# Kernel optimization log

Hardware: AMD Instinct MI355X
Metric: run time of the kernel (lower is better)

The kernel has to match this reference:

```python
import jax, jax.numpy as jnp
import numpy as np

TEMPERATURE = 8.0  # sqrt(head_dim=64)


def setup_inputs() -> dict:
    key = jax.random.key(0)
    ks = jax.random.split(key, 6)
    B, H, S, D = 8, 8, 1024, 64
    shp = (B, H, S, D)
    names = ["q_r", "q_i", "k_r", "k_i", "v_r", "v_i"]
    return {n: jax.random.normal(k, shp, dtype=jnp.float32) for n, k in zip(names, ks)}


def _mag_minmax_norm(attn):
    """cvnn.MagMinMaxNorm(dim=-1): min-max normalize the magnitude along the
    last axis while preserving phase: x * (|x| - min) / ((max - min) * |x|)."""
    mag = jnp.abs(attn)                              # [B,H,Sq,Sk] real
    mn = jnp.min(mag, axis=-1, keepdims=True)
    mx = jnp.max(mag, axis=-1, keepdims=True)
    return attn * ((mag - mn) / ((mx - mn) * mag))


def reference(q_r, q_i, k_r, k_i, v_r, v_i):
    q = jax.lax.complex(q_r, q_i)
    k = jax.lax.complex(k_r, k_i)
    v = jax.lax.complex(v_r, v_i)
    # complex QK^T with temperature scaling
    attn = jnp.einsum("bhqd,bhkd->bhqk", q / TEMPERATURE, k)
    attn = _mag_minmax_norm(attn)
    # dropout is identity at inference (eval mode)
    out = jnp.einsum("bhqk,bhkd->bhqd", attn, v)
    # return real/imag stacked: [2, B, H, S, D]
    return jnp.stack([out.real, out.imag])
```

## Files before the change

### kernel.cpp

```cpp
#include <hip/hip_runtime.h>
#include <math.h>

typedef unsigned short ushort_t;
typedef __attribute__((ext_vector_type(8))) short short8;
typedef __attribute__((ext_vector_type(4))) float f32x4;
typedef __attribute__((ext_vector_type(4))) int int4v;
typedef __attribute__((ext_vector_type(4))) unsigned short ushort4v;

constexpr int S = 1024, D = 64, BH = 64;
constexpr int HALF = BH * S * D;
constexpr int KROW = 72;
constexpr int VROW = 40;
constexpr int TILE_USH = 2 * 32 * KROW + 2 * 64 * VROW;
constexpr size_t WS_NEED = (size_t)BH * 32 * TILE_USH * 2;

#define MFMA16(a, b, c) __builtin_amdgcn_mfma_f32_16x16x32_bf16(a, b, c, 0, 0, 0)

__device__ __forceinline__ ushort_t f2bf(float f) {
  unsigned u = __float_as_uint(f);
  u += 0x7fff + ((u >> 16) & 1);
  return (ushort_t)(u >> 16);
}

__global__ __launch_bounds__(256)
void prepass_kernel(const float* __restrict__ kr, const float* __restrict__ ki,
                    const float* __restrict__ vr, const float* __restrict__ vi,
                    ushort_t* __restrict__ ws) {
  __shared__ float tmp2[32 * 65];
  const int t = threadIdx.x;
  const int tile = blockIdx.x;
  const size_t gbase = (size_t)tile * (32 * D);
  ushort_t* wst = ws + (size_t)tile * TILE_USH;

  const int k = t >> 3, d0 = (t & 7) * 8;
  {
    const float* kp[2] = {kr, ki};
#pragma unroll
    for (int c = 0; c < 2; ++c) {
      const float* src = kp[c] + gbase + k * D + d0;
      float4 a = *(const float4*)src;
      float4 b = *(const float4*)(src + 4);
      ushort4v w0 = {f2bf(a.x), f2bf(a.y), f2bf(a.z), f2bf(a.w)};
      ushort4v w1 = {f2bf(b.x), f2bf(b.y), f2bf(b.z), f2bf(b.w)};
      ushort_t* dst = wst + c * (32 * KROW) + k * KROW + d0;
      *(ushort4v*)dst = w0;
      *(ushort4v*)(dst + 4) = w1;
    }
  }
  const float* vp[2] = {vr, vi};
  for (int c = 0; c < 2; ++c) {
    if (c) __syncthreads();
    {
      const float* src = vp[c] + gbase + k * D + d0;
      float4 a = *(const float4*)src;
      float4 b = *(const float4*)(src + 4);
      *(float4*)&tmp2[k * 65 + d0] = a;
      *(float4*)&tmp2[k * 65 + d0 + 4] = b;
    }
    __syncthreads();
    const int d = t >> 2, k0 = (t & 3) * 8;
    float v[8];
#pragma unroll
    for (int j = 0; j < 8; ++j) v[j] = tmp2[(k0 + j) * 65 + d];
    ushort4v o0 = {f2bf(v[0]), f2bf(v[1]), f2bf(v[2]), f2bf(v[3])};
    ushort4v o1 = {f2bf(v[4]), f2bf(v[5]), f2bf(v[6]), f2bf(v[7])};
    ushort_t* dst = wst + 2 * (32 * KROW) + c * (64 * VROW) + d * VROW + k0;
    *(ushort4v*)dst = o0;
    *(ushort4v*)(dst + 4) = o1;
  }
}

__global__ __launch_bounds__(256, 2)
void cvattn_mfma(const float* __restrict__ gq_r, const float* __restrict__ gq_i,
                 const ushort_t* __restrict__ ws, float* __restrict__ gout) {
  __shared__ __attribute__((aligned(16))) char smem[39936];
  ushort_t* sB = (ushort_t*)smem;
  ushort_t* sP = (ushort_t*)(smem + 19456);
  ushort_t* sQ = (ushort_t*)(smem + 19456);

  const int t = threadIdx.x;
  const int lane = t & 63, wave = t >> 6;
  const int m = lane & 15, quad = lane >> 4;
  const int qt = blockIdx.x, bh = blockIdx.y;
  const size_t base = (size_t)bh * (S * D);

  {
    const float* qr = gq_r + base + (size_t)qt * (64 * D);
    const float* qi = gq_i + base + (size_t)qt * (64 * D);
#pragma unroll
    for (int i = 0; i < 4; ++i) {
      int e = (i * 256 + t) * 4;
      int q = e >> 6, d = e & 63;
      float4 a = *(const float4*)(qr + e);
      float4 b = *(const float4*)(qi + e);
      ushort4v wa = {f2bf(a.x), f2bf(a.y), f2bf(a.z), f2bf(a.w)};
      ushort4v wb = {f2bf(b.x), f2bf(b.y), f2bf(b.z), f2bf(b.w)};
      *(ushort4v*)&sQ[q * KROW + d] = wa;
      *(ushort4v*)&sQ[64 * KROW + q * KROW + d] = wb;
    }
  }
  __syncthreads();

  short8 fQr[2], fQi[2], fQin[2];
  {
    const int qrow = wave * 16 + m;
#pragma unroll
    for (int dc = 0; dc < 2; ++dc) {
      fQr[dc] = *(const short8*)&sQ[qrow * KROW + dc * 32 + quad * 8];
      fQi[dc] = *(const short8*)&sQ[64 * KROW + qrow * KROW + dc * 32 + quad * 8];
      fQin[dc] = fQi[dc] ^ (short)0x8000;
    }
  }

  f32x4 aAr[4] = {}, aAi[4] = {}, aUr[4] = {}, aUi[4] = {};
  float mn4[4] = {1e30f, 1e30f, 1e30f, 1e30f};
  float mx4[4] = {0.f, 0.f, 0.f, 0.f};

  ushort_t* pw = sP + wave * 2560;
  const ushort_t* wsrc = ws + (size_t)bh * 32 * TILE_USH;

  int4v pre[5];
#pragma unroll
  for (int i = 0; i < 5; ++i) {
    int idx = i * 256 + t;
    if (idx < 1216) pre[i] = *(const int4v*)(wsrc + idx * 8);
  }

  for (int kb = 0; kb < 32; ++kb) {
    __syncthreads();
#pragma unroll
    for (int i = 0; i < 5; ++i) {
      int idx = i * 256 + t;
      if (idx < 1216) *(int4v*)(smem + idx * 16) = pre[i];
    }
    if (kb + 1 < 32) {
      const ushort_t* g = wsrc + (size_t)(kb + 1) * TILE_USH;
#pragma unroll
      for (int i = 0; i < 5; ++i) {
        int idx = i * 256 + t;
        if (idx < 1216) pre[i] = *(const int4v*)(g + idx * 8);
      }
    }
    __syncthreads();

#pragma unroll
    for (int ks = 0; ks < 2; ++ks) {
      const int krow = ks * 16 + m;
      short8 fKr0 = *(const short8*)&sB[krow * KROW + quad * 8];
      short8 fKr1 = *(const short8*)&sB[krow * KROW + 32 + quad * 8];
      short8 fKi0 = *(const short8*)&sB[2304 + krow * KROW + quad * 8];
      short8 fKi1 = *(const short8*)&sB[2304 + krow * KROW + 32 + quad * 8];
      f32x4 cSr = {}, cSi = {};
      cSr = MFMA16(fQr[0], fKr0, cSr);
      cSr = MFMA16(fQr[1], fKr1, cSr);
      cSr = MFMA16(fQin[0], fKi0, cSr);
      cSr = MFMA16(fQin[1], fKi1, cSr);
      cSi = MFMA16(fQr[0], fKi0, cSi);
      cSi = MFMA16(fQr[1], fKi1, cSi);
      cSi = MFMA16(fQi[0], fKr0, cSi);
      cSi = MFMA16(fQi[1], fKr1, cSi);
      const int pcol = ((ks * 2 + (m >> 3)) ^ quad) * 8 + (m & 7);
#pragma unroll
      for (int r = 0; r < 4; ++r) {
        float sr = cSr[r], si = cSi[r];
        float t2 = sr * sr + si * si;
        float rq = __builtin_amdgcn_rsqf(t2);
        mn4[r] = fminf(mn4[r], t2);
        mx4[r] = fmaxf(mx4[r], t2);
        const int off = (quad * 4 + r) * VROW + pcol;
        pw[off] = f2bf(sr);
        pw[640 + off] = f2bf(si);
        pw[1280 + off] = f2bf(sr * rq);
        pw[1920 + off] = f2bf(si * rq);
      }
    }

    const int prow = m * VROW + ((quad ^ (m >> 2)) * 8);
    short8 fPr = *(const short8*)&pw[prow];
    short8 fPi = *(const short8*)&pw[640 + prow];
    short8 fUr = *(const short8*)&pw[1280 + prow];
    short8 fUi = *(const short8*)&pw[1920 + prow];
#pragma unroll
    for (int dt = 0; dt < 4; ++dt) {
      const int drow = dt * 16 + m;
      short8 fVr = *(const short8*)&sB[4608 + drow * VROW + quad * 8];
      short8 fVi = *(const short8*)&sB[7168 + drow * VROW + quad * 8];
      short8 fVin = fVi ^ (short)0x8000;
      aAr[dt] = MFMA16(fPr, fVr, aAr[dt]);
      aAr[dt] = MFMA16(fPi, fVin, aAr[dt]);
      aAi[dt] = MFMA16(fPr, fVi, aAi[dt]);
      aAi[dt] = MFMA16(fPi, fVr, aAi[dt]);
      aUr[dt] = MFMA16(fUr, fVr, aUr[dt]);
      aUr[dt] = MFMA16(fUi, fVin, aUr[dt]);
      aUi[dt] = MFMA16(fUr, fVi, aUi[dt]);
      aUi[dt] = MFMA16(fUi, fVr, aUi[dt]);
    }
  }

#pragma unroll
  for (int r = 0; r < 4; ++r) {
#pragma unroll
    for (int mask = 1; mask < 16; mask <<= 1) {
      mn4[r] = fminf(mn4[r], __shfl_xor(mn4[r], mask, 64));
      mx4[r] = fmaxf(mx4[r], __shfl_xor(mx4[r], mask, 64));
    }
  }
  float inv[4];
#pragma unroll
  for (int r = 0; r < 4; ++r) {
    mn4[r] = sqrtf(mn4[r]);
    mx4[r] = sqrtf(mx4[r]);
    inv[r] = 1.0f / (mx4[r] - mn4[r]);
  }

  const int qbase = qt * 64 + wave * 16 + quad * 4;
#pragma unroll
  for (int dt = 0; dt < 4; ++dt) {
    const int d = dt * 16 + m;
#pragma unroll
    for (int r = 0; r < 4; ++r) {
      size_t o = base + (size_t)(qbase + r) * D + d;
      gout[o] = (aAr[dt][r] - mn4[r] * aUr[dt][r]) * inv[r];
      gout[HALF + o] = (aAi[dt][r] - mn4[r] * aUi[dt][r]) * inv[r];
    }
  }
}

constexpr int QT = 32, KT = 32;
constexpr int DP = D + 4;
constexpr int KP = KT + 1;

#define CDOT4(SR, SI, AR, AI, BR, BI)                              \
  SR += AR.x*BR.x + AR.y*BR.y + AR.z*BR.z + AR.w*BR.w              \
      - AI.x*BI.x - AI.y*BI.y - AI.z*BI.z - AI.w*BI.w;             \
  SI += AR.x*BI.x + AR.y*BI.y + AR.z*BI.z + AR.w*BI.w              \
      + AI.x*BR.x + AI.y*BR.y + AI.z*BR.z + AI.w*BR.w;

__global__ __launch_bounds__(256, 2)
void cvattn_fallback(const float* __restrict__ gq_r, const float* __restrict__ gq_i,
                     const float* __restrict__ gk_r, const float* __restrict__ gk_i,
                     const float* __restrict__ gv_r, const float* __restrict__ gv_i,
                     float* __restrict__ gout) {
  __shared__ float qs_r[QT][DP], qs_i[QT][DP];
  __shared__ float ks_r[KT][DP], ks_i[KT][DP];
  __shared__ float vs_r[KT][DP], vs_i[KT][DP];
  __shared__ float sc_r[QT][KP], sc_i[QT][KP], sc_m[QT][KP];
  const int t = threadIdx.x;
  const int qt2 = blockIdx.x, bh = blockIdx.y;
  const size_t base = (size_t)bh * (S * D);
  {
    const float* qr_p = gq_r + base + (size_t)qt2 * QT * D;
    const float* qi_p = gq_i + base + (size_t)qt2 * QT * D;
#pragma unroll
    for (int i = 0; i < 2; ++i) {
      int e = (t + i * 256) * 4;
      int row = e >> 6, col = e & 63;
      *(float4*)&qs_r[row][col] = *(const float4*)(qr_p + e);
      *(float4*)&qs_i[row][col] = *(const float4*)(qi_p + e);
    }
  }
  const int q0 = (t >> 4) * 2, k0 = (t & 15) * 2;
  const int rB = t >> 3, dc = (t & 7) * 8;
  float Ar[8] = {}, Ai[8] = {}, Ur[8] = {}, Ui[8] = {};
  float mn = 3.4e38f, mx = 0.0f;
  for (int kb = 0; kb < S / KT; ++kb) {
    __syncthreads();
    {
      const float* kr_p = gk_r + base + (size_t)kb * KT * D;
      const float* ki_p = gk_i + base + (size_t)kb * KT * D;
      const float* vr_p = gv_r + base + (size_t)kb * KT * D;
      const float* vi_p = gv_i + base + (size_t)kb * KT * D;
#pragma unroll
    for (int i = 0; i < 2; ++i) {
        int e = (t + i * 256) * 4;
        int row = e >> 6, col = e & 63;
        *(float4*)&ks_r[row][col] = *(const float4*)(kr_p + e);
        *(float4*)&ks_i[row][col] = *(const float4*)(ki_p + e);
        *(float4*)&vs_r[row][col] = *(const float4*)(vr_p + e);
        *(float4*)&vs_i[row][col] = *(const float4*)(vi_p + e);
      }
    }
    __syncthreads();
    {
      float s00r=0.f,s00i=0.f,s01r=0.f,s01i=0.f;
      float s10r=0.f,s10i=0.f,s11r=0.f,s11i=0.f;
#pragma unroll
      for (int d = 0; d < D; d += 4) {
        float4 a0r = *(const float4*)&qs_r[q0  ][d];
        float4 a0i = *(const float4*)&qs_i[q0  ][d];
        float4 a1r = *(const float4*)&qs_r[q0+1][d];
        float4 a1i = *(const float4*)&qs_i[q0+1][d];
        float4 b0r = *(const float4*)&ks_r[k0  ][d];
        float4 b0i = *(const float4*)&ks_i[k0  ][d];
        float4 b1r = *(const float4*)&ks_r[k0+1][d];
        float4 b1i = *(const float4*)&ks_i[k0+1][d];
        CDOT4(s00r, s00i, a0r, a0i, b0r, b0i);
        CDOT4(s01r, s01i, a0r, a0i, b1r, b1i);
        CDOT4(s10r, s10i, a1r, a1i, b0r, b0i);
        CDOT4(s11r, s11i, a1r, a1i, b1r, b1i);
      }
      s00r *= 0.125f; s00i *= 0.125f; s01r *= 0.125f; s01i *= 0.125f;
      s10r *= 0.125f; s10i *= 0.125f; s11r *= 0.125f; s11i *= 0.125f;
      sc_r[q0  ][k0  ] = s00r; sc_i[q0  ][k0  ] = s00i;
      sc_m[q0  ][k0  ] = sqrtf(s00r*s00r + s00i*s00i);
      sc_r[q0  ][k0+1] = s01r; sc_i[q0  ][k0+1] = s01i;
      sc_m[q0  ][k0+1] = sqrtf(s01r*s01r + s01i*s01i);
      sc_r[q0+1][k0  ] = s10r; sc_i[q0+1][k0  ] = s10i;
      sc_m[q0+1][k0  ] = sqrtf(s10r*s10r + s10i*s10i);
      sc_r[q0+1][k0+1] = s11r; sc_i[q0+1][k0+1] = s11i;
      sc_m[q0+1][k0+1] = sqrtf(s11r*s11r + s11i*s11i);
    }
    __syncthreads();
#pragma unroll 8
    for (int k = 0; k < KT; ++k) {
      float sr = sc_r[rB][k], si = sc_i[rB][k], mg = sc_m[rB][k];
      mn = fminf(mn, mg); mx = fmaxf(mx, mg);
      float inv = 1.0f / mg;
      float ur = sr * inv, ui = si * inv;
      float vr[8], vi[8];
      *(float4*)&vr[0] = *(const float4*)&vs_r[k][dc];
      *(float4*)&vr[4] = *(const float4*)&vs_r[k][dc + 4];
      *(float4*)&vi[0] = *(const float4*)&vs_i[k][dc];
      *(float4*)&vi[4] = *(const float4*)&vs_i[k][dc + 4];
#pragma unroll
      for (int j = 0; j < 8; ++j) {
        Ar[j] += sr * vr[j] - si * vi[j];
        Ai[j] += sr * vi[j] + si * vr[j];
        Ur[j] += ur * vr[j] - ui * vi[j];
        Ui[j] += ur * vi[j] + ui * vr[j];
      }
    }
  }
  float invspan = 1.0f / (mx - mn);
  float outr[8], outi[8];
#pragma unroll
  for (int j = 0; j < 8; ++j) {
    outr[j] = (Ar[j] - mn * Ur[j]) * invspan;
    outi[j] = (Ai[j] - mn * Ui[j]) * invspan;
  }
  size_t o = base + (size_t)(qt2 * QT + rB) * D + dc;
  *(float4*)(gout + o)            = *(float4*)&outr[0];
  *(float4*)(gout + o + 4)        = *(float4*)&outr[4];
  *(float4*)(gout + HALF + o)     = *(float4*)&outi[0];
  *(float4*)(gout + HALF + o + 4) = *(float4*)&outi[4];
}

extern "C" void kernel_launch(void* const* d_in, const int* in_sizes, int n_in,
                              void* d_out, int out_size, void* d_ws, size_t ws_size,
                              hipStream_t stream) {
  if (ws_size >= WS_NEED) {
    prepass_kernel<<<dim3(BH * 32), 256, 0, stream>>>(
        (const float*)d_in[2], (const float*)d_in[3],
        (const float*)d_in[4], (const float*)d_in[5], (ushort_t*)d_ws);
    cvattn_mfma<<<dim3(S / 64, BH), 256, 0, stream>>>(
        (const float*)d_in[0], (const float*)d_in[1],
        (const ushort_t*)d_ws, (float*)d_out);
  } else {
    cvattn_fallback<<<dim3(S / QT, BH), 256, 0, stream>>>(
        (const float*)d_in[0], (const float*)d_in[1],
        (const float*)d_in[2], (const float*)d_in[3],
        (const float*)d_in[4], (const float*)d_in[5], (float*)d_out);
  }
}
```

Measured before the change: 263.6 us.

## Double-buffer K/V tiles via direct global-to-LDS loads and pack P stores

```diff
diff --git a/kernel.cpp b/kernel.cpp
--- a/kernel.cpp
+++ b/kernel.cpp
@@ -5,13 +5,13 @@
 typedef __attribute__((ext_vector_type(8))) short short8;
 typedef __attribute__((ext_vector_type(4))) float f32x4;
 typedef __attribute__((ext_vector_type(4))) int int4v;
-typedef __attribute__((ext_vector_type(4))) unsigned short ushort4v;
 
 constexpr int S = 1024, D = 64, BH = 64;
 constexpr int HALF = BH * S * D;
 constexpr int KROW = 72;
 constexpr int VROW = 40;
 constexpr int TILE_USH = 2 * 32 * KROW + 2 * 64 * VROW;
+constexpr int TILE_B = TILE_USH * 2;
 constexpr size_t WS_NEED = (size_t)BH * 32 * TILE_USH * 2;
 
 #define MFMA16(a, b, c) __builtin_amdgcn_mfma_f32_16x16x32_bf16(a, b, c, 0, 0, 0)
@@ -20,6 +20,15 @@
   unsigned u = __float_as_uint(f);
   u += 0x7fff + ((u >> 16) & 1);
   return (ushort_t)(u >> 16);
+}
+
+__device__ __forceinline__ int4v pack8(float4 a, float4 b) {
+  int4v r;
+  r.x = (unsigned)f2bf(a.x) | ((unsigned)f2bf(a.y) << 16);
+  r.y = (unsigned)f2bf(a.z) | ((unsigned)f2bf(a.w) << 16);
+  r.z = (unsigned)f2bf(b.x) | ((unsigned)f2bf(b.y) << 16);
+  r.w = (unsigned)f2bf(b.z) | ((unsigned)f2bf(b.w) << 16);
+  return r;
 }
 
 __global__ __launch_bounds__(256)
@@ -31,52 +40,78 @@
   const int tile = blockIdx.x;
   const size_t gbase = (size_t)tile * (32 * D);
   ushort_t* wst = ws + (size_t)tile * TILE_USH;
-
   const int k = t >> 3, d0 = (t & 7) * 8;
-  {
-    const float* kp[2] = {kr, ki};
-#pragma unroll
-    for (int c = 0; c < 2; ++c) {
-      const float* src = kp[c] + gbase + k * D + d0;
-      float4 a = *(const float4*)src;
-      float4 b = *(const float4*)(src + 4);
-      ushort4v w0 = {f2bf(a.x), f2bf(a.y), f2bf(a.z), f2bf(a.w)};
-      ushort4v w1 = {f2bf(b.x), f2bf(b.y), f2bf(b.z), f2bf(b.w)};
-      ushort_t* dst = wst + c * (32 * KROW) + k * KROW + d0;
-      *(ushort4v*)dst = w0;
-      *(ushort4v*)(dst + 4) = w1;
-    }
-  }
-  const float* vp[2] = {vr, vi};
-  for (int c = 0; c < 2; ++c) {
-    if (c) __syncthreads();
-    {
-      const float* src = vp[c] + gbase + k * D + d0;
-      float4 a = *(const float4*)src;
-      float4 b = *(const float4*)(src + 4);
-      *(float4*)&tmp2[k * 65 + d0] = a;
-      *(float4*)&tmp2[k * 65 + d0 + 4] = b;
-    }
-    __syncthreads();
-    const int d = t >> 2, k0 = (t & 3) * 8;
-    float v[8];
-#pragma unroll
-    for (int j = 0; j < 8; ++j) v[j] = tmp2[(k0 + j) * 65 + d];
-    ushort4v o0 = {f2bf(v[0]), f2bf(v[1]), f2bf(v[2]), f2bf(v[3])};
-    ushort4v o1 = {f2bf(v[4]), f2bf(v[5]), f2bf(v[6]), f2bf(v[7])};
-    ushort_t* dst = wst + 2 * (32 * KROW) + c * (64 * VROW) + d * VROW + k0;
-    *(ushort4v*)dst = o0;
-    *(ushort4v*)(dst + 4) = o1;
-  }
+  const int dT = t >> 2, k0 = (t & 3) * 8;
+
+  {
+    float4 a = *(const float4*)(kr + gbase + k * D + d0);
+    float4 b = *(const float4*)(kr + gbase + k * D + d0 + 4);
+    *(int4v*)(wst + k * KROW + d0) = pack8(a, b);
+  }
+  {
+    float4 a = *(const float4*)(ki + gbase + k * D + d0);
+    float4 b = *(const float4*)(ki + gbase + k * D + d0 + 4);
+    *(int4v*)(wst + 2304 + k * KROW + d0) = pack8(a, b);
+  }
+  {
+    float4 a = *(const float4*)(vr + gbase + k * D + d0);
+    float4 b = *(const float4*)(vr + gbase + k * D + d0 + 4);
+    *(float4*)&tmp2[k * 65 + d0] = a;
+    *(float4*)&tmp2[k * 65 + d0 + 4] = b;
+  }
+  __syncthreads();
+  {
+    float4 a, b;
+    a.x = tmp2[(k0 + 0) * 65 + dT]; a.y = tmp2[(k0 + 1) * 65 + dT];
+    a.z = tmp2[(k0 + 2) * 65 + dT]; a.w = tmp2[(k0 + 3) * 65 + dT];
+    b.x = tmp2[(k0 + 4) * 65 + dT]; b.y = tmp2[(k0 + 5) * 65 + dT];
+    b.z = tmp2[(k0 + 6) * 65 + dT]; b.w = tmp2[(k0 + 7) * 65 + dT];
+    *(int4v*)(wst + 4608 + dT * VROW + k0) = pack8(a, b);
+  }
+  __syncthreads();
+  {
+    float4 a = *(const float4*)(vi + gbase + k * D + d0);
+    float4 b = *(const float4*)(vi + gbase + k * D + d0 + 4);
+    *(float4*)&tmp2[k * 65 + d0] = a;
+    *(float4*)&tmp2[k * 65 + d0 + 4] = b;
+  }
+  __syncthreads();
+  {
+    float4 a, b;
+    a.x = tmp2[(k0 + 0) * 65 + dT]; a.y = tmp2[(k0 + 1) * 65 + dT];
+    a.z = tmp2[(k0 + 2) * 65 + dT]; a.w = tmp2[(k0 + 3) * 65 + dT];
+    b.x = tmp2[(k0 + 4) * 65 + dT]; b.y = tmp2[(k0 + 5) * 65 + dT];
+    b.z = tmp2[(k0 + 6) * 65 + dT]; b.w = tmp2[(k0 + 7) * 65 + dT];
+    *(int4v*)(wst + 4608 + 64 * VROW + dT * VROW + k0) = pack8(a, b);
+  }
+}
+
+__device__ __forceinline__ void stage_tile_async(const ushort_t* __restrict__ g,
+                                                 char* dst, int t) {
+#if __has_builtin(__builtin_amdgcn_global_load_lds)
+#pragma unroll
+  for (int i = 0; i < 5; ++i) {
+    int idx = i * 256 + t;
+    if (idx < TILE_B / 16)
+      __builtin_amdgcn_global_load_lds(
+          (const __attribute__((address_space(1))) unsigned int*)(g + idx * 8),
+          (__attribute__((address_space(3))) unsigned int*)(dst + idx * 16),
+          16, 0, 0);
+  }
+#else
+#pragma unroll
+  for (int i = 0; i < 5; ++i) {
+    int idx = i * 256 + t;
+    if (idx < TILE_B / 16) *(int4v*)(dst + idx * 16) = *(const int4v*)(g + idx * 8);
+  }
+#endif
 }
 
 __global__ __launch_bounds__(256, 2)
 void cvattn_mfma(const float* __restrict__ gq_r, const float* __restrict__ gq_i,
                  const ushort_t* __restrict__ ws, float* __restrict__ gout) {
-  __shared__ __attribute__((aligned(16))) char smem[39936];
-  ushort_t* sB = (ushort_t*)smem;
-  ushort_t* sP = (ushort_t*)(smem + 19456);
-  ushort_t* sQ = (ushort_t*)(smem + 19456);
+  __shared__ __attribute__((aligned(16))) char smem[59392];
+  ushort_t* sQ = (ushort_t*)(smem + 38912);
 
   const int t = threadIdx.x;
   const int lane = t & 63, wave = t >> 6;
@@ -93,10 +128,10 @@
       int q = e >> 6, d = e & 63;
       float4 a = *(const float4*)(qr + e);
       float4 b = *(const float4*)(qi + e);
-      ushort4v wa = {f2bf(a.x), f2bf(a.y), f2bf(a.z), f2bf(a.w)};
-      ushort4v wb = {f2bf(b.x), f2bf(b.y), f2bf(b.z), f2bf(b.w)};
-      *(ushort4v*)&sQ[q * KROW + d] = wa;
-      *(ushort4v*)&sQ[64 * KROW + q * KROW + d] = wb;
+      ushort_t* pa = &sQ[q * KROW + d];
+      ushort_t* pb = &sQ[64 * KROW + q * KROW + d];
+      pa[0] = f2bf(a.x); pa[1] = f2bf(a.y); pa[2] = f2bf(a.z); pa[3] = f2bf(a.w);
+      pb[0] = f2bf(b.x); pb[1] = f2bf(b.y); pb[2] = f2bf(b.z); pb[3] = f2bf(b.w);
     }
   }
   __syncthreads();
@@ -116,40 +151,26 @@
   float mn4[4] = {1e30f, 1e30f, 1e30f, 1e30f};
   float mx4[4] = {0.f, 0.f, 0.f, 0.f};
 
-  ushort_t* pw = sP + wave * 2560;
+  unsigned* pwu = (unsigned*)(smem + 38912) + wave * 1280;
+  ushort_t* pw = (ushort_t*)pwu;
   const ushort_t* wsrc = ws + (size_t)bh * 32 * TILE_USH;
 
-  int4v pre[5];
-#pragma unroll
-  for (int i = 0; i < 5; ++i) {
-    int idx = i * 256 + t;
-    if (idx < 1216) pre[i] = *(const int4v*)(wsrc + idx * 8);
-  }
+  stage_tile_async(wsrc, smem, t);
 
   for (int kb = 0; kb < 32; ++kb) {
     __syncthreads();
-#pragma unroll
-    for (int i = 0; i < 5; ++i) {
-      int idx = i * 256 + t;
-      if (idx < 1216) *(int4v*)(smem + idx * 16) = pre[i];
-    }
-    if (kb + 1 < 32) {
-      const ushort_t* g = wsrc + (size_t)(kb + 1) * TILE_USH;
-#pragma unroll
-      for (int i = 0; i < 5; ++i) {
-        int idx = i * 256 + t;
-        if (idx < 1216) pre[i] = *(const int4v*)(g + idx * 8);
-      }
-    }
-    __syncthreads();
+    if (kb + 1 < 32)
+      stage_tile_async(wsrc + (size_t)(kb + 1) * TILE_USH, smem + ((kb + 1) & 1) * TILE_B, t);
+
+    const ushort_t* cb = (const ushort_t*)(smem + (kb & 1) * TILE_B);
 
 #pragma unroll
     for (int ks = 0; ks < 2; ++ks) {
       const int krow = ks * 16 + m;
-      short8 fKr0 = *(const short8*)&sB[krow * KROW + quad * 8];
-      short8 fKr1 = *(const short8*)&sB[krow * KROW + 32 + quad * 8];
-      short8 fKi0 = *(const short8*)&sB[2304 + krow * KROW + quad * 8];
-      short8 fKi1 = *(const short8*)&sB[2304 + krow * KROW + 32 + quad * 8];
+      short8 fKr0 = *(const short8*)&cb[krow * KROW + quad * 8];
+      short8 fKr1 = *(const short8*)&cb[krow * KROW + 32 + quad * 8];
+      short8 fKi0 = *(const short8*)&cb[2304 + krow * KROW + quad * 8];
+      short8 fKi1 = *(const short8*)&cb[2304 + krow * KROW + 32 + quad * 8];
       f32x4 cSr = {}, cSi = {};
       cSr = MFMA16(fQr[0], fKr0, cSr);
       cSr = MFMA16(fQr[1], fKr1, cSr);
@@ -159,7 +180,8 @@
       cSi = MFMA16(fQr[1], fKi1, cSi);
       cSi = MFMA16(fQi[0], fKr0, cSi);
       cSi = MFMA16(fQi[1], fKr1, cSi);
-      const int pcol = ((ks * 2 + (m >> 3)) ^ quad) * 8 + (m & 7);
+      const int cphys = (ks * 8 + (m >> 1)) ^ ((quad & 2) << 2);
+      const bool evenm = (m & 1) == 0;
 #pragma unroll
       for (int r = 0; r < 4; ++r) {
         float sr = cSr[r], si = cSi[r];
@@ -167,15 +189,23 @@
         float rq = __builtin_amdgcn_rsqf(t2);
         mn4[r] = fminf(mn4[r], t2);
         mx4[r] = fmaxf(mx4[r], t2);
-        const int off = (quad * 4 + r) * VROW + pcol;
-        pw[off] = f2bf(sr);
-        pw[640 + off] = f2bf(si);
-        pw[1280 + off] = f2bf(sr * rq);
-        pw[1920 + off] = f2bf(si * rq);
+        unsigned psr = f2bf(sr), psi = f2bf(si);
+        unsigned pur = f2bf(sr * rq), pui = f2bf(si * rq);
+        unsigned nsr = __shfl_xor((int)psr, 1, 64);
+        unsigned nsi = __shfl_xor((int)psi, 1, 64);
+        unsigned nur = __shfl_xor((int)pur, 1, 64);
+        unsigned nui = __shfl_xor((int)pui, 1, 64);
+        if (evenm) {
+          int dwo = (quad * 4 + r) * 20 + cphys;
+          pwu[dwo]       = psr | (nsr << 16);
+          pwu[320 + dwo] = psi | (nsi << 16);
+          pwu[640 + dwo] = pur | (nur << 16);
+          pwu[960 + dwo] = pui | (nui << 16);
+        }
       }
     }
 
-    const int prow = m * VROW + ((quad ^ (m >> 2)) * 8);
+    const int prow = m * VROW + ((quad * 8) ^ ((m & 8) << 1));
     short8 fPr = *(const short8*)&pw[prow];
     short8 fPi = *(const short8*)&pw[640 + prow];
     short8 fUr = *(const short8*)&pw[1280 + prow];
@@ -183,8 +213,8 @@
 #pragma unroll
     for (int dt = 0; dt < 4; ++dt) {
       const int drow = dt * 16 + m;
-      short8 fVr = *(const short8*)&sB[4608 + drow * VROW + quad * 8];
-      short8 fVi = *(const short8*)&sB[7168 + drow * VROW + quad * 8];
+      short8 fVr = *(const short8*)&cb[4608 + drow * VROW + quad * 8];
+      short8 fVi = *(const short8*)&cb[7168 + drow * VROW + quad * 8];
       short8 fVin = fVi ^ (short)0x8000;
       aAr[dt] = MFMA16(fPr, fVr, aAr[dt]);
       aAr[dt] = MFMA16(fPi, fVin, aAr[dt]);
@@ -271,7 +301,7 @@
       const float* vr_p = gv_r + base + (size_t)kb * KT * D;
       const float* vi_p = gv_i + base + (size_t)kb * KT * D;
 #pragma unroll
-    for (int i = 0; i < 2; ++i) {
+      for (int i = 0; i < 2; ++i) {
         int e = (t + i * 256) * 4;
         int row = e >> 6, col = e & 63;
         *(float4*)&ks_r[row][col] = *(const float4*)(kr_p + e);
```

Measured after the change: 303.5 us. 15.1% more time.
